# Kernel tuning notes

Measured on AMD Instinct MI355X. Metric: run time of the kernel, lower is better.

## Reference

```python
import jax, jax.numpy as jnp
import numpy as np

NB, H = 4, 8          # blocks, heads
B, S = 2, 1024        # batch, seq
D, HID = 512, 512     # input_dim, hidden_dim (must match, see zeros_like(x) branch)
# mod computed from neurochem BEFORE _modulate_neurochem, using init values
MOD = 0.5 * 1.1 + 0.5 * 0.7 + 0.5 * 1.3 - 0.0 * 1.2  # = 1.55


def setup_inputs() -> dict:
    key = jax.random.key(0)
    ks = jax.random.split(key, 12)
    sc = 1.0 / np.sqrt(D)
    inp = {
        "x": jax.random.normal(ks[0], (B, S, D), jnp.float32),
        "Wq": jax.random.normal(ks[1], (NB, D, HID), jnp.float32) * sc,
        "bq": jax.random.normal(ks[2], (NB, HID), jnp.float32) * sc,
        "Wk": jax.random.normal(ks[3], (NB, D, HID), jnp.float32) * sc,
        "bk": jax.random.normal(ks[4], (NB, HID), jnp.float32) * sc,
        "Wv": jax.random.normal(ks[5], (NB, D, HID), jnp.float32) * sc,
        "bv": jax.random.normal(ks[6], (NB, HID), jnp.float32) * sc,
        "Wo": jax.random.normal(ks[7], (NB, HID, D), jnp.float32) * sc,
        "bo": jax.random.normal(ks[8], (NB, D), jnp.float32) * sc,
        "strength": jax.random.uniform(ks[9], (NB, H, H), jnp.float32),
        # gate = (osc_mask * spike_mask > 0.5) materialized as 0/1 floats
        "gate": (jax.random.uniform(ks[10], (NB, H)) < 0.7).astype(jnp.float32),
    }
    return inp


def reference(x, Wq, bq, Wk, bk, Wv, bv, Wo, bo, strength, gate):
    # per-block projections (shared across heads in the original loop)
    q = jnp.einsum('bsd,ndh->nbsh', x, Wq) + bq[:, None, None, :]
    k = jnp.einsum('bsd,ndh->nbsh', x, Wk) + bk[:, None, None, :]
    v = jnp.einsum('bsd,ndh->nbsh', x, Wv) + bv[:, None, None, :]
    scores = jnp.einsum('nbsh,nbth->nbst', q, k) / jnp.sqrt(jnp.float32(HID))
    # per-head scalar bias: diagonal synaptic strength, clamped
    s = jnp.clip(jnp.diagonal(strength, axis1=1, axis2=2), 0.01, 1.0)  # [NB, H]
    scaled = scores[:, None] * s[:, :, None, None, None]  # [NB, H, B, S, S]
    probs = jax.nn.softmax(scaled, axis=-1)
    # head outputs summed with the 0/1 osc*spike gate
    head_sum = jnp.einsum('nhbst,nbtd,nh->nbsd', probs, v, gate)  # [NB, B, S, HID]
    block_out = jnp.einsum('nbsd,ndo->nbso', head_sum, Wo) + bo[:, None, None, :]
    return block_out.sum(axis=0) * jnp.float32(MOD)
```

## Files before the change

kernel.cpp:

```cpp
#include <hip/hip_runtime.h>
#include <math.h>

#define NBLK   4
#define NH     8
#define BATCH  2
#define SEQ    1024
#define DIM    512
#define HIDDEN 512
#define MODF   1.55f
#define INV_SQRT_HID 0.04419417382415922f

typedef __bf16 bf16;
typedef __bf16 bf16x4 __attribute__((ext_vector_type(4)));
typedef __bf16 bf16x8 __attribute__((ext_vector_type(8)));
typedef float  floatx4 __attribute__((ext_vector_type(4)));

constexpr int BM = 128, BN = 128, BK = 32;

__device__ __forceinline__ void load16_lds(const bf16* g, bf16* l) {
    __builtin_amdgcn_global_load_lds(
        (__attribute__((address_space(1))) void*)g,
        (__attribute__((address_space(3))) void*)l, 16, 0, 0);
}

__device__ __forceinline__ void mfma_nt(
    const bf16* __restrict__ A, int lda,
    const bf16* __restrict__ B, int ldb,
    int K, int m0, int n0, floatx4 (&acc)[4][4])
{
    __shared__ __align__(16) bf16 As[BM * BK];
    __shared__ __align__(16) bf16 Bs[BN * BK];

    const int tid = threadIdx.x;
    const int l   = tid & 63;
    const int w   = tid >> 6;
    const int wr  = (w >> 1) * 64;
    const int wc  = (w & 1) * 64;

    const int s0 = 2 * w, s1 = s0 + 1;
    const int r0 = s0 * 16 + (l >> 2);
    const int r1 = s1 * 16 + (l >> 2);
    const int kc = (l & 3) * 8;

    const int fr = l & 15;
    const int fk = (l >> 4) * 8;

    const bf16* Ab = A + (size_t)m0 * lda;
    const bf16* Bb = B + (size_t)n0 * ldb;

    for (int k0 = 0; k0 < K; k0 += BK) {
        __syncthreads();
        load16_lds(Ab + (size_t)r0 * lda + k0 + kc, As + s0 * 512);
        load16_lds(Ab + (size_t)r1 * lda + k0 + kc, As + s1 * 512);
        load16_lds(Bb + (size_t)r0 * ldb + k0 + kc, Bs + s0 * 512);
        load16_lds(Bb + (size_t)r1 * ldb + k0 + kc, Bs + s1 * 512);
        __syncthreads();

        bf16x8 af[4], bg[4];
#pragma unroll
        for (int i = 0; i < 4; ++i)
            af[i] = *(const bf16x8*)&As[(wr + i * 16 + fr) * BK + fk];
#pragma unroll
        for (int j = 0; j < 4; ++j)
            bg[j] = *(const bf16x8*)&Bs[(wc + j * 16 + fr) * BK + fk];
#pragma unroll
        for (int i = 0; i < 4; ++i)
#pragma unroll
            for (int j = 0; j < 4; ++j)
                acc[i][j] = __builtin_amdgcn_mfma_f32_16x16x32_bf16(
                    af[i], bg[j], acc[i][j], 0, 0, 0);
    }
}

__global__ __launch_bounds__(256) void xconv_kernel(
    const float* __restrict__ x, bf16* __restrict__ xb)
{
    const int t = blockIdx.x * 256 + threadIdx.x;
    const float4 v = ((const float4*)x)[t];
    bf16x4 o = { (bf16)v.x, (bf16)v.y, (bf16)v.z, (bf16)v.w };
    *(bf16x4*)&xb[(size_t)t * 4] = o;
}

__global__ __launch_bounds__(256) void transpose_w_kernel(
    const float* __restrict__ Wq, const float* __restrict__ Wk,
    const float* __restrict__ Wv, const float* __restrict__ Wo,
    bf16* __restrict__ WqT, bf16* __restrict__ WkT,
    bf16* __restrict__ WvT, bf16* __restrict__ WoT)
{
    __shared__ float tile[32][33];
    const int z = blockIdx.z;
    const int mat = z >> 2, n = z & 3;
    const float* src; bf16* dst;
    if (mat == 0)      { src = Wq; dst = WqT; }
    else if (mat == 1) { src = Wk; dst = WkT; }
    else if (mat == 2) { src = Wv; dst = WvT; }
    else               { src = Wo; dst = WoT; }
    src += (size_t)n * 512 * 512;
    dst += (size_t)n * 512 * 512;

    const int tx = threadIdx.x & 31, ty = threadIdx.x >> 5;
    const int x0 = blockIdx.x * 32, y0 = blockIdx.y * 32;
#pragma unroll
    for (int r = 0; r < 4; ++r)
        tile[ty + r * 8][tx] = src[(size_t)(y0 + ty + r * 8) * 512 + x0 + tx];
    __syncthreads();
#pragma unroll
    for (int r = 0; r < 4; ++r)
        dst[(size_t)(x0 + ty + r * 8) * 512 + y0 + tx] = (bf16)tile[tx][ty + r * 8];
}

__global__ __launch_bounds__(256) void transpose_v_kernel(
    const bf16* __restrict__ Vm, bf16* __restrict__ Vt)
{
    __shared__ float tile[32][33];
    const int z = blockIdx.z;
    const bf16* src = Vm + (size_t)z * SEQ * HIDDEN;
    bf16*       dst = Vt + (size_t)z * HIDDEN * SEQ;

    const int tx = threadIdx.x & 31, ty = threadIdx.x >> 5;
    const int x0 = blockIdx.x * 32;
    const int y0 = blockIdx.y * 32;
#pragma unroll
    for (int r = 0; r < 4; ++r)
        tile[ty + r * 8][tx] = (float)src[(size_t)(y0 + ty + r * 8) * HIDDEN + x0 + tx];
    __syncthreads();
#pragma unroll
    for (int r = 0; r < 4; ++r)
        dst[(size_t)(x0 + ty + r * 8) * SEQ + y0 + tx] = (bf16)tile[tx][ty + r * 8];
}

__global__ __launch_bounds__(256) void proj_mfma_kernel(
    const bf16* __restrict__ xb,
    const bf16* __restrict__ WqT, const bf16* __restrict__ WkT,
    const bf16* __restrict__ WvT,
    const float* __restrict__ bq, const float* __restrict__ bk,
    const float* __restrict__ bv,
    bf16* __restrict__ Qh, bf16* __restrict__ Kh, bf16* __restrict__ Vm)
{
    const int z = blockIdx.z;
    const int n = z & 3, which = z >> 2;
    const bf16* WT; const float* bias; bf16* Cb;
    if (which == 0)      { WT = WqT; bias = bq; Cb = Qh; }
    else if (which == 1) { WT = WkT; bias = bk; Cb = Kh; }
    else                 { WT = WvT; bias = bv; Cb = Vm; }
    WT   += (size_t)n * DIM * HIDDEN;
    bias += (size_t)n * HIDDEN;
    bf16* C = Cb + (size_t)n * (BATCH * SEQ) * HIDDEN;

    const int m0 = blockIdx.y * BM, n0 = blockIdx.x * BN;
    floatx4 acc[4][4] = {};
    mfma_nt(xb, DIM, WT, DIM, DIM, m0, n0, acc);

    const int l = threadIdx.x & 63, w = threadIdx.x >> 6;
    const int rb = m0 + (w >> 1) * 64 + (l >> 4) * 4;
    const int cb = n0 + (w & 1) * 64 + (l & 15);
#pragma unroll
    for (int j = 0; j < 4; ++j) {
        const int col = cb + j * 16;
        const float bc = bias[col];
#pragma unroll
        for (int i = 0; i < 4; ++i)
#pragma unroll
            for (int r = 0; r < 4; ++r)
                C[(size_t)(rb + i * 16 + r) * HIDDEN + col] = (bf16)(acc[i][j][r] + bc);
    }
}

__global__ __launch_bounds__(256) void scores_mfma_kernel(
    const bf16* __restrict__ Qh, const bf16* __restrict__ Kh,
    float* __restrict__ P)
{
    const int z = blockIdx.z;
    const bf16* A = Qh + (size_t)z * SEQ * HIDDEN;
    const bf16* B = Kh + (size_t)z * SEQ * HIDDEN;
    float* C = P + (size_t)z * SEQ * SEQ;

    const int m0 = blockIdx.y * BM, n0 = blockIdx.x * BN;
    floatx4 acc[4][4] = {};
    mfma_nt(A, HIDDEN, B, HIDDEN, HIDDEN, m0, n0, acc);

    const int l = threadIdx.x & 63, w = threadIdx.x >> 6;
    const int rb = m0 + (w >> 1) * 64 + (l >> 4) * 4;
    const int cb = n0 + (w & 1) * 64 + (l & 15);
#pragma unroll
    for (int i = 0; i < 4; ++i)
#pragma unroll
        for (int j = 0; j < 4; ++j)
#pragma unroll
            for (int r = 0; r < 4; ++r)
                C[(size_t)(rb + i * 16 + r) * SEQ + cb + j * 16] =
                    acc[i][j][r] * INV_SQRT_HID;
}

__global__ __launch_bounds__(256) void softmax_combine_kernel(
    const float* __restrict__ P, bf16* __restrict__ Pb,
    const float* __restrict__ strength, const float* __restrict__ gate)
{
    const int row = blockIdx.x;
    const int n = row >> 11;
    const float* prow = P + (size_t)row * SEQ;
    const int tid = threadIdx.x;
    const int wid = tid >> 6, lane = tid & 63;

    float4 v = ((const float4*)prow)[tid];

    float m = fmaxf(fmaxf(v.x, v.y), fmaxf(v.z, v.w));
#pragma unroll
    for (int off = 32; off > 0; off >>= 1) m = fmaxf(m, __shfl_down(m, off));
    __shared__ float redm[4];
    if (lane == 0) redm[wid] = m;
    __syncthreads();
    const float M = fmaxf(fmaxf(redm[0], redm[1]), fmaxf(redm[2], redm[3]));

    float sh[NH], gh[NH];
#pragma unroll
    for (int h = 0; h < NH; ++h) {
        sh[h] = fminf(fmaxf(strength[n * NH * NH + h * NH + h], 0.01f), 1.0f);
        gh[h] = gate[n * NH + h];
    }

    const float e[4] = { v.x - M, v.y - M, v.z - M, v.w - M };
    float E[4][NH];
    float zsum[NH];
#pragma unroll
    for (int h = 0; h < NH; ++h) zsum[h] = 0.f;
#pragma unroll
    for (int i = 0; i < 4; ++i)
#pragma unroll
        for (int h = 0; h < NH; ++h) {
            const float t = __expf(sh[h] * e[i]);
            E[i][h] = t; zsum[h] += t;
        }

#pragma unroll
    for (int h = 0; h < NH; ++h)
#pragma unroll
        for (int off = 32; off > 0; off >>= 1) zsum[h] += __shfl_down(zsum[h], off);
    __shared__ float redz[4][NH];
    if (lane == 0)
#pragma unroll
        for (int h = 0; h < NH; ++h) redz[wid][h] = zsum[h];
    __syncthreads();

    float wgt[NH];
#pragma unroll
    for (int h = 0; h < NH; ++h) {
        const float Z = redz[0][h] + redz[1][h] + redz[2][h] + redz[3][h];
        wgt[h] = gh[h] / Z;
    }

    bf16x4 o;
#pragma unroll
    for (int i = 0; i < 4; ++i) {
        float s = 0.f;
#pragma unroll
        for (int h = 0; h < NH; ++h) s += wgt[h] * E[i][h];
        o[i] = (bf16)s;
    }
    *(bf16x4*)&Pb[(size_t)row * SEQ + tid * 4] = o;
}

__global__ __launch_bounds__(256) void pv_mfma_kernel(
    const bf16* __restrict__ Pb, const bf16* __restrict__ Vt,
    bf16* __restrict__ HS)
{
    const int z = blockIdx.z;
    const bf16* A = Pb + (size_t)z * SEQ * SEQ;
    const bf16* B = Vt + (size_t)z * HIDDEN * SEQ;
    bf16* C = HS + (size_t)z * SEQ * HIDDEN;

    const int m0 = blockIdx.y * BM, n0 = blockIdx.x * BN;
    floatx4 acc[4][4] = {};
    mfma_nt(A, SEQ, B, SEQ, SEQ, m0, n0, acc);

    const int l = threadIdx.x & 63, w = threadIdx.x >> 6;
    const int rb = m0 + (w >> 1) * 64 + (l >> 4) * 4;
    const int cb = n0 + (w & 1) * 64 + (l & 15);
#pragma unroll
    for (int i = 0; i < 4; ++i)
#pragma unroll
        for (int j = 0; j < 4; ++j)
#pragma unroll
            for (int r = 0; r < 4; ++r)
                C[(size_t)(rb + i * 16 + r) * HIDDEN + cb + j * 16] =
                    (bf16)acc[i][j][r];
}

__global__ __launch_bounds__(256) void out_partial_kernel(
    const bf16* __restrict__ HS, const bf16* __restrict__ WoT,
    float* __restrict__ Opart)
{
    const int n = blockIdx.z;
    const bf16* A = HS + (size_t)n * (BATCH * SEQ) * HIDDEN;
    const bf16* B = WoT + (size_t)n * HIDDEN * DIM;
    float* C = Opart + (size_t)n * (BATCH * SEQ) * DIM;

    const int m0 = blockIdx.y * BM, n0 = blockIdx.x * BN;
    floatx4 acc[4][4] = {};
    mfma_nt(A, HIDDEN, B, HIDDEN, HIDDEN, m0, n0, acc);

    const int l = threadIdx.x & 63, w = threadIdx.x >> 6;
    const int rb = m0 + (w >> 1) * 64 + (l >> 4) * 4;
    const int cb = n0 + (w & 1) * 64 + (l & 15);
#pragma unroll
    for (int i = 0; i < 4; ++i)
#pragma unroll
        for (int j = 0; j < 4; ++j)
#pragma unroll
            for (int r = 0; r < 4; ++r)
                C[(size_t)(rb + i * 16 + r) * DIM + cb + j * 16] = acc[i][j][r];
}

__global__ __launch_bounds__(256) void out_reduce_kernel(
    const float* __restrict__ Opart, const float* __restrict__ bo,
    float* __restrict__ out)
{
    const size_t t = (size_t)blockIdx.x * 256 + threadIdx.x;
    const int c = (int)((t * 4) & (DIM - 1));
    const size_t stride4 = (size_t)(BATCH * SEQ) * DIM / 4;

    float4 s = ((const float4*)Opart)[t];
#pragma unroll
    for (int n = 1; n < NBLK; ++n) {
        const float4 p = ((const float4*)Opart)[t + n * stride4];
        s.x += p.x; s.y += p.y; s.z += p.z; s.w += p.w;
    }
    float4 bs = make_float4(0.f, 0.f, 0.f, 0.f);
#pragma unroll
    for (int n = 0; n < NBLK; ++n) {
        const float4 b = *(const float4*)(bo + n * DIM + c);
        bs.x += b.x; bs.y += b.y; bs.z += b.z; bs.w += b.w;
    }
    ((float4*)out)[t] = make_float4((s.x + bs.x) * MODF, (s.y + bs.y) * MODF,
                                    (s.z + bs.z) * MODF, (s.w + bs.w) * MODF);
}

extern "C" void kernel_launch(void* const* d_in, const int* in_sizes, int n_in,
                              void* d_out, int out_size, void* d_ws, size_t ws_size,
                              hipStream_t stream) {
    const float* x        = (const float*)d_in[0];
    const float* Wq       = (const float*)d_in[1];
    const float* bq       = (const float*)d_in[2];
    const float* Wk       = (const float*)d_in[3];
    const float* bk       = (const float*)d_in[4];
    const float* Wv       = (const float*)d_in[5];
    const float* bv       = (const float*)d_in[6];
    const float* Wo       = (const float*)d_in[7];
    const float* bo       = (const float*)d_in[8];
    const float* strength = (const float*)d_in[9];
    const float* gate     = (const float*)d_in[10];
    float* out = (float*)d_out;

    char* ws = (char*)d_ws;
    bf16*  xb    = (bf16*)(ws);
    bf16*  WqT   = (bf16*)(ws + (2u  << 20));
    bf16*  WkT   = (bf16*)(ws + (4u  << 20));
    bf16*  WvT   = (bf16*)(ws + (6u  << 20));
    bf16*  WoT   = (bf16*)(ws + (8u  << 20));
    bf16*  Qh    = (bf16*)(ws + (10u << 20));
    bf16*  Kh    = (bf16*)(ws + (18u << 20));
    bf16*  Vm    = (bf16*)(ws + (26u << 20));
    bf16*  Vt    = (bf16*)(ws + (34u << 20));
    float* Pf    = (float*)(ws + (42u << 20));
    bf16*  Pb    = (bf16*)(ws + (10u << 20));
    bf16*  HS    = (bf16*)(ws + (26u << 20));
    float* Opart = (float*)(ws + (42u << 20));

    xconv_kernel<<<dim3((BATCH * SEQ * DIM) / 1024), 256, 0, stream>>>(x, xb);
    transpose_w_kernel<<<dim3(16, 16, 16), 256, 0, stream>>>(
        Wq, Wk, Wv, Wo, WqT, WkT, WvT, WoT);

    proj_mfma_kernel<<<dim3(HIDDEN / BN, (BATCH * SEQ) / BM, 3 * NBLK), 256, 0, stream>>>(
        xb, WqT, WkT, WvT, bq, bk, bv, Qh, Kh, Vm);

    transpose_v_kernel<<<dim3(HIDDEN / 32, SEQ / 32, NBLK * BATCH), 256, 0, stream>>>(
        Vm, Vt);

    scores_mfma_kernel<<<dim3(SEQ / BN, SEQ / BM, NBLK * BATCH), 256, 0, stream>>>(
        Qh, Kh, Pf);

    softmax_combine_kernel<<<dim3(NBLK * BATCH * SEQ), 256, 0, stream>>>(
        Pf, Pb, strength, gate);

    pv_mfma_kernel<<<dim3(HIDDEN / BN, SEQ / BM, NBLK * BATCH), 256, 0, stream>>>(
        Pb, Vt, HS);

    out_partial_kernel<<<dim3(DIM / BN, (BATCH * SEQ) / BM, NBLK), 256, 0, stream>>>(
        HS, WoT, Opart);

    out_reduce_kernel<<<dim3((BATCH * SEQ) * DIM / 4 / 256), 256, 0, stream>>>(
        Opart, bo, out);
}
```

Before: 204.3 us.

## Double-buffer MFMA GEMM LDS tiles and fuse V transpose into projection epilogue

Measured after the change: 194.2 us. 1.05x faster.

```diff
diff --git a/kernel.cpp b/kernel.cpp
--- a/kernel.cpp
+++ b/kernel.cpp
@@ -23,52 +23,72 @@
         (__attribute__((address_space(3))) void*)l, 16, 0, 0);
 }
 
+__device__ __forceinline__ void stage32(
+    const bf16* __restrict__ Ab, int lda,
+    const bf16* __restrict__ Bb, int ldb, int k0,
+    bf16* As, bf16* Bs, int w, int l)
+{
+    const int s0 = 2 * w, s1 = s0 + 1;
+    const int r0 = s0 * 16 + (l >> 2);
+    const int r1 = s1 * 16 + (l >> 2);
+    const int kc = (l & 3) * 8;
+    load16_lds(Ab + (size_t)r0 * lda + k0 + kc, As + s0 * 512);
+    load16_lds(Ab + (size_t)r1 * lda + k0 + kc, As + s1 * 512);
+    load16_lds(Bb + (size_t)r0 * ldb + k0 + kc, Bs + s0 * 512);
+    load16_lds(Bb + (size_t)r1 * ldb + k0 + kc, Bs + s1 * 512);
+}
+
+__device__ __forceinline__ void comp32(
+    const bf16* As, const bf16* Bs,
+    int wr, int wc, int fr, int fk, floatx4 (&acc)[4][4])
+{
+    bf16x8 af[4], bg[4];
+#pragma unroll
+    for (int i = 0; i < 4; ++i)
+        af[i] = *(const bf16x8*)&As[(wr + i * 16 + fr) * BK + fk];
+#pragma unroll
+    for (int j = 0; j < 4; ++j)
+        bg[j] = *(const bf16x8*)&Bs[(wc + j * 16 + fr) * BK + fk];
+#pragma unroll
+    for (int i = 0; i < 4; ++i)
+#pragma unroll
+        for (int j = 0; j < 4; ++j)
+            acc[i][j] = __builtin_amdgcn_mfma_f32_16x16x32_bf16(
+                af[i], bg[j], acc[i][j], 0, 0, 0);
+}
+
 __device__ __forceinline__ void mfma_nt(
     const bf16* __restrict__ A, int lda,
     const bf16* __restrict__ B, int ldb,
     int K, int m0, int n0, floatx4 (&acc)[4][4])
 {
-    __shared__ __align__(16) bf16 As[BM * BK];
-    __shared__ __align__(16) bf16 Bs[BN * BK];
+    __shared__ __align__(16) bf16 As0[BM * BK];
+    __shared__ __align__(16) bf16 Bs0[BN * BK];
+    __shared__ __align__(16) bf16 As1[BM * BK];
+    __shared__ __align__(16) bf16 Bs1[BN * BK];
 
     const int tid = threadIdx.x;
     const int l   = tid & 63;
     const int w   = tid >> 6;
     const int wr  = (w >> 1) * 64;
     const int wc  = (w & 1) * 64;
-
-    const int s0 = 2 * w, s1 = s0 + 1;
-    const int r0 = s0 * 16 + (l >> 2);
-    const int r1 = s1 * 16 + (l >> 2);
-    const int kc = (l & 3) * 8;
-
-    const int fr = l & 15;
-    const int fk = (l >> 4) * 8;
+    const int fr  = l & 15;
+    const int fk  = (l >> 4) * 8;
 
     const bf16* Ab = A + (size_t)m0 * lda;
     const bf16* Bb = B + (size_t)n0 * ldb;
 
-    for (int k0 = 0; k0 < K; k0 += BK) {
+    const int nIter = K / BK;
+    stage32(Ab, lda, Bb, ldb, 0, As0, Bs0, w, l);
+    for (int k = 0; k < nIter; k += 2) {
         __syncthreads();
-        load16_lds(Ab + (size_t)r0 * lda + k0 + kc, As + s0 * 512);
-        load16_lds(Ab + (size_t)r1 * lda + k0 + kc, As + s1 * 512);
-        load16_lds(Bb + (size_t)r0 * ldb + k0 + kc, Bs + s0 * 512);
-        load16_lds(Bb + (size_t)r1 * ldb + k0 + kc, Bs + s1 * 512);
+        if (k + 1 < nIter)
+            stage32(Ab, lda, Bb, ldb, (k + 1) * BK, As1, Bs1, w, l);
+        comp32(As0, Bs0, wr, wc, fr, fk, acc);
         __syncthreads();
-
-        bf16x8 af[4], bg[4];
-#pragma unroll
-        for (int i = 0; i < 4; ++i)
-            af[i] = *(const bf16x8*)&As[(wr + i * 16 + fr) * BK + fk];
-#pragma unroll
-        for (int j = 0; j < 4; ++j)
-            bg[j] = *(const bf16x8*)&Bs[(wc + j * 16 + fr) * BK + fk];
-#pragma unroll
-        for (int i = 0; i < 4; ++i)
-#pragma unroll
-            for (int j = 0; j < 4; ++j)
-                acc[i][j] = __builtin_amdgcn_mfma_f32_16x16x32_bf16(
-                    af[i], bg[j], acc[i][j], 0, 0, 0);
+        if (k + 2 < nIter)
+            stage32(Ab, lda, Bb, ldb, (k + 2) * BK, As0, Bs0, w, l);
+        comp32(As1, Bs1, wr, wc, fr, fk, acc);
     }
 }
 
@@ -109,43 +129,22 @@
         dst[(size_t)(x0 + ty + r * 8) * 512 + y0 + tx] = (bf16)tile[tx][ty + r * 8];
 }
 
-__global__ __launch_bounds__(256) void transpose_v_kernel(
-    const bf16* __restrict__ Vm, bf16* __restrict__ Vt)
-{
-    __shared__ float tile[32][33];
-    const int z = blockIdx.z;
-    const bf16* src = Vm + (size_t)z * SEQ * HIDDEN;
-    bf16*       dst = Vt + (size_t)z * HIDDEN * SEQ;
-
-    const int tx = threadIdx.x & 31, ty = threadIdx.x >> 5;
-    const int x0 = blockIdx.x * 32;
-    const int y0 = blockIdx.y * 32;
-#pragma unroll
-    for (int r = 0; r < 4; ++r)
-        tile[ty + r * 8][tx] = (float)src[(size_t)(y0 + ty + r * 8) * HIDDEN + x0 + tx];
-    __syncthreads();
-#pragma unroll
-    for (int r = 0; r < 4; ++r)
-        dst[(size_t)(x0 + ty + r * 8) * SEQ + y0 + tx] = (bf16)tile[tx][ty + r * 8];
-}
-
 __global__ __launch_bounds__(256) void proj_mfma_kernel(
     const bf16* __restrict__ xb,
     const bf16* __restrict__ WqT, const bf16* __restrict__ WkT,
     const bf16* __restrict__ WvT,
     const float* __restrict__ bq, const float* __restrict__ bk,
     const float* __restrict__ bv,
-    bf16* __restrict__ Qh, bf16* __restrict__ Kh, bf16* __restrict__ Vm)
+    bf16* __restrict__ Qh, bf16* __restrict__ Kh, bf16* __restrict__ Vt)
 {
     const int z = blockIdx.z;
     const int n = z & 3, which = z >> 2;
-    const bf16* WT; const float* bias; bf16* Cb;
-    if (which == 0)      { WT = WqT; bias = bq; Cb = Qh; }
-    else if (which == 1) { WT = WkT; bias = bk; Cb = Kh; }
-    else                 { WT = WvT; bias = bv; Cb = Vm; }
+    const bf16* WT; const float* bias;
+    if (which == 0)      { WT = WqT; bias = bq; }
+    else if (which == 1) { WT = WkT; bias = bk; }
+    else                 { WT = WvT; bias = bv; }
     WT   += (size_t)n * DIM * HIDDEN;
     bias += (size_t)n * HIDDEN;
-    bf16* C = Cb + (size_t)n * (BATCH * SEQ) * HIDDEN;
 
     const int m0 = blockIdx.y * BM, n0 = blockIdx.x * BN;
     floatx4 acc[4][4] = {};
@@ -154,15 +153,34 @@
     const int l = threadIdx.x & 63, w = threadIdx.x >> 6;
     const int rb = m0 + (w >> 1) * 64 + (l >> 4) * 4;
     const int cb = n0 + (w & 1) * 64 + (l & 15);
-#pragma unroll
-    for (int j = 0; j < 4; ++j) {
-        const int col = cb + j * 16;
-        const float bc = bias[col];
-#pragma unroll
-        for (int i = 0; i < 4; ++i)
-#pragma unroll
-            for (int r = 0; r < 4; ++r)
-                C[(size_t)(rb + i * 16 + r) * HIDDEN + col] = (bf16)(acc[i][j][r] + bc);
+
+    if (which != 2) {
+        bf16* C = (which ? Kh : Qh) + (size_t)n * (BATCH * SEQ) * HIDDEN;
+#pragma unroll
+        for (int j = 0; j < 4; ++j) {
+            const int col = cb + j * 16;
+            const float bc = bias[col];
+#pragma unroll
+            for (int i = 0; i < 4; ++i)
+#pragma unroll
+                for (int r = 0; r < 4; ++r)
+                    C[(size_t)(rb + i * 16 + r) * HIDDEN + col] = (bf16)(acc[i][j][r] + bc);
+        }
+    } else {
+        const int b = m0 >> 10;
+        bf16* Cv = Vt + (size_t)(n * BATCH + b) * HIDDEN * SEQ;
+        const int tb = rb & (SEQ - 1);
+#pragma unroll
+        for (int j = 0; j < 4; ++j) {
+            const int col = cb + j * 16;
+            const float bc = bias[col];
+#pragma unroll
+            for (int i = 0; i < 4; ++i) {
+                bf16x4 o = { (bf16)(acc[i][j][0] + bc), (bf16)(acc[i][j][1] + bc),
+                             (bf16)(acc[i][j][2] + bc), (bf16)(acc[i][j][3] + bc) };
+                *(bf16x4*)&Cv[(size_t)col * SEQ + tb + i * 16] = o;
+            }
+        }
     }
 }
 
@@ -359,11 +377,10 @@
     bf16*  WoT   = (bf16*)(ws + (8u  << 20));
     bf16*  Qh    = (bf16*)(ws + (10u << 20));
     bf16*  Kh    = (bf16*)(ws + (18u << 20));
-    bf16*  Vm    = (bf16*)(ws + (26u << 20));
-    bf16*  Vt    = (bf16*)(ws + (34u << 20));
-    float* Pf    = (float*)(ws + (42u << 20));
+    bf16*  Vt    = (bf16*)(ws + (26u << 20));
+    float* Pf    = (float*)(ws + (34u << 20));
     bf16*  Pb    = (bf16*)(ws + (10u << 20));
-    bf16*  HS    = (bf16*)(ws + (26u << 20));
+    bf16*  HS    = (bf16*)(ws + (34u << 20));
     float* Opart = (float*)(ws + (42u << 20));
 
     xconv_kernel<<<dim3((BATCH * SEQ * DIM) / 1024), 256, 0, stream>>>(x, xb);
@@ -371,10 +388,7 @@
         Wq, Wk, Wv, Wo, WqT, WkT, WvT, WoT);
 
     proj_mfma_kernel<<<dim3(HIDDEN / BN, (BATCH * SEQ) / BM, 3 * NBLK), 256, 0, stream>>>(
-        xb, WqT, WkT, WvT, bq, bk, bv, Qh, Kh, Vm);
-
-    transpose_v_kernel<<<dim3(HIDDEN / 32, SEQ / 32, NBLK * BATCH), 256, 0, stream>>>(
-        Vm, Vt);
+        xb, WqT, WkT, WvT, bq, bk, bv, Qh, Kh, Vt);
 
     scores_mfma_kernel<<<dim3(SEQ / BN, SEQ / BM, NBLK * BATCH), 256, 0, stream>>>(
         Qh, Kh, Pf);
```
